# Optimization experiments

Hardware: AMD Instinct MI355X
Metric: run time of the kernel (lower is better)

## Reference

```python
import jax, jax.numpy as jnp
import numpy as np

B, M, D, V = 2048, 64, 256, 50000  # batch, max neighbors, embed dim, num_symbols (pad idx = V)
EPS = 1e-5


def _ln(x, g, b):
    mu = jnp.mean(x, axis=-1, keepdims=True)
    var = jnp.var(x, axis=-1, keepdims=True)
    return (x - mu) * jax.lax.rsqrt(var + EPS) * g + b


def _attn(q, k, v, Wq, Wk, Wv, Wb, Wo, bo):
    # q: (B, D); k, v: (B, M, D). num_heads=1, att_size=D. NOTE: self.scale is defined
    # but never used in the original forward, so no scaling here (faithful).
    qh = q @ Wq.T                                   # (B, D)
    kh = jnp.einsum('bmd,ed->bme', k, Wk)           # (B, M, D)
    vh = jnp.einsum('bmd,ed->bme', v, Wv)           # (B, M, D)
    s = jnp.einsum('bd,bmd->bm', qh @ Wb.T, kh)     # bilinear-modulated scores
    a = jax.nn.softmax(s, axis=-1)
    o = jnp.einsum('bm,bmd->bd', a, vh)
    return o @ Wo.T + bo


def setup_inputs() -> dict:
    key = jax.random.key(0)
    ks = jax.random.split(key, 40)
    f = lambda i, shape, s=0.05: (jax.random.normal(ks[i], shape, dtype=jnp.float32) * s)
    emb = f(0, (V + 1, D), 0.1).at[V].set(0.0)  # padding_idx row is zero
    inp = {
        'entity_pairs': jax.random.randint(ks[1], (B, 2), 0, V),
        'left_conn': jax.random.randint(ks[2], (B, M, 2), 0, V),
        'left_deg': jax.random.randint(ks[3], (B,), 0, M),
        'right_conn': jax.random.randint(ks[4], (B, M, 2), 0, V),
        'right_deg': jax.random.randint(ks[5], (B,), 0, M),
        'emb': emb,
        # task-aware attention params
        'Wq_t': f(6, (D, D)), 'Wk_t': f(7, (D, D)), 'Wv_t': f(8, (D, D)),
        'Wbil_t': f(9, (D, D)), 'Wo_t': f(10, (D, D)), 'bo_t': jnp.zeros((D,), jnp.float32),
        # entity-pair attention params
        'Wq_e': f(11, (D, D)), 'Wk_e': f(12, (D, D)), 'Wv_e': f(13, (D, D)),
        'Wbil_e': f(14, (D, D)), 'Wo_e': f(15, (D, D)), 'bo_e': jnp.zeros((D,), jnp.float32),
        'ln_g': jnp.ones((D,), jnp.float32), 'ln_b': jnp.zeros((D,), jnp.float32),
        'Wtail': f(16, (D, D)), 'Whead': f(17, (D, D)),
        'Wrel': f(18, (2 * D, D, D), 0.02),  # nn.Bilinear weight (out, in1, in2), no bias
        'W1': f(19, (2 * D, 2 * D)), 'b1': jnp.zeros((2 * D,), jnp.float32),
        'W2': f(20, (2 * D, 2 * D)),
        'ln1_g': jnp.ones((2 * D,), jnp.float32), 'ln1_b': jnp.zeros((2 * D,), jnp.float32),
        'Wg': f(21, (D, D), 0.3), 'Ug': f(22, (D, D), 0.3), 'bg': jnp.zeros((D,), jnp.float32),
        'Wr': f(23, (D, D), 0.3), 'Ur': f(24, (D, D), 0.3), 'br': jnp.zeros((D,), jnp.float32),
    }
    return inp


def reference(entity_pairs, left_conn, left_deg, right_conn, right_deg, emb,
              Wq_t, Wk_t, Wv_t, Wbil_t, Wo_t, bo_t,
              Wq_e, Wk_e, Wv_e, Wbil_e, Wo_e, bo_e,
              ln_g, ln_b, Wtail, Whead, Wrel, W1, b1, W2, ln1_g, ln1_b,
              Wg, Ug, bg, Wr, Ur, br):
    # eval mode: dropouts are identity
    ent = emb[entity_pairs]                 # (B, 2, D)
    eL, eR = ent[:, 0], ent[:, 1]           # (B, D) each
    rel_L = emb[left_conn[:, :, 0]]         # (B, M, D)
    ent_L = emb[left_conn[:, :, 1]]
    rel_R = emb[right_conn[:, :, 0]]
    ent_R = emb[right_conn[:, :, 1]]

    # rel_w bilinear: (B, 2D) -> split into forward/backward task relation embeddings
    rel_emb = jnp.einsum('bi,oij,bj->bo', eL, Wrel, eR)
    rel_fwd, rel_bwd = rel_emb[:, :D], rel_emb[:, D:]

    # GRU-style neighbor gating
    g = jax.nn.sigmoid(rel_L @ Wg + ent_L @ Ug + bg)
    V_head = jax.nn.relu(g * rel_L + (1.0 - g) * ent_L)
    gr = jax.nn.sigmoid(rel_R @ Wr + ent_R @ Ur + br)
    V_tail = jax.nn.relu(gr * rel_R + (1.0 - gr) * ent_R)

    def enhance(att_out, e):
        h = jax.nn.relu(att_out @ Wtail.T + e @ Whead.T)
        return _ln(h + e, ln_g, ln_b)

    h_rel = _attn(rel_fwd, rel_L, V_head, Wq_t, Wk_t, Wv_t, Wbil_t, Wo_t, bo_t)
    enh_head_ = enhance(h_rel, eL)
    t_rel = _attn(rel_bwd, rel_R, V_tail, Wq_t, Wk_t, Wv_t, Wbil_t, Wo_t, bo_t)
    enh_tail_ = enhance(t_rel, eR)

    h_ent = _attn(enh_tail_, ent_L, V_head, Wq_e, Wk_e, Wv_e, Wbil_e, Wo_e, bo_e)
    enh_head = enhance(h_ent, eL)
    t_ent = _attn(enh_head_, ent_R, V_tail, Wq_e, Wk_e, Wv_e, Wbil_e, Wo_e, bo_e)
    enh_tail = enhance(t_ent, eR)

    pair = jnp.concatenate([enh_head, enh_tail], axis=-1)  # (B, 2D)
    # bi_MLP with residual + LayerNorm
    h = jax.nn.relu(pair @ W1.T + b1)
    h = h @ W2.T
    return _ln(h + pair, ln1_g, ln1_b)
```

## Files before the change

kernel.cpp:

```cpp
#include <hip/hip_runtime.h>
#include <hip/hip_bf16.h>

#define BN 2048
#define MN 64
#define DN 256
#define EMB_ROWS 50001
#define EMB_PAD 50016
#define LN_EPS 1e-5f
#define SPLITK 16
#define KCHUNK 4096

typedef __hip_bfloat16 bf16;
typedef __attribute__((ext_vector_type(8))) short bf16x8;
typedef __attribute__((ext_vector_type(4))) float f32x4;

static __device__ __forceinline__ short f2bf(float f) {
  return __builtin_bit_cast(short, __float2bfloat16(f));
}
static __device__ __forceinline__ float bfu(unsigned short u) {
  unsigned int x = ((unsigned int)u) << 16;
  return __builtin_bit_cast(float, x);
}

typedef __attribute__((address_space(1))) const void g_void;
typedef __attribute__((address_space(3))) void l_void;
static __device__ __forceinline__ void gl_lds16(const void* g, void* l) {
  __builtin_amdgcn_global_load_lds((g_void*)g, (l_void*)l, 16, 0, 0);
}

static __device__ __forceinline__ void dev_mm(float* __restrict__ C, const float* __restrict__ A,
                                              const float* __restrict__ B, int N, int K,
                                              int aI, int aM, int bM, int bJ, int blk, int tid) {
  int idx = blk * 256 + tid;
  int i = idx / N, j = idx - i * N;
  float s = 0.f;
  for (int m = 0; m < K; ++m) s += A[i * aI + m * aM] * B[m * bM + j * bJ];
  C[idx] = s;
}
static __device__ __forceinline__ void dev_tr(float* __restrict__ dst, const float* __restrict__ src,
                                              int rows, int cols, int blk, int tid) {
  int idx = blk * 256 + tid;
  int r = idx / cols, c = idx - r * cols;
  dst[c * rows + r] = src[idx];
}

#define S1_GRID 27349
__global__ void k_stage1(const float* __restrict__ Wbil_t, const float* __restrict__ Wq_t,
                         const float* __restrict__ Wbil_e, const float* __restrict__ Wq_e,
                         const float* __restrict__ Wo_t, const float* __restrict__ Wv_t,
                         const float* __restrict__ Wo_e, const float* __restrict__ Wv_e,
                         const float* __restrict__ Wtail, const float* __restrict__ Whead,
                         const float* __restrict__ W1, const float* __restrict__ W2,
                         const float* __restrict__ Wg, const float* __restrict__ Ug,
                         const float* __restrict__ Wr, const float* __restrict__ Ur,
                         const float* __restrict__ Wrel, const float* __restrict__ emb,
                         const int* __restrict__ pairs,
                         float* __restrict__ T_t, float* __restrict__ T_e,
                         float* __restrict__ Wov_t, float* __restrict__ Wov_e,
                         float* __restrict__ WtailT, float* __restrict__ Whead_kn,
                         float* __restrict__ W1_kn, float* __restrict__ W2_kn,
                         bf16* __restrict__ wcat, bf16* __restrict__ emb_bf,
                         float* __restrict__ eL, float* __restrict__ eR,
                         bf16* __restrict__ eRbf, float* __restrict__ eLT,
                         bf16* __restrict__ Wrel_bf) {
  int bid = blockIdx.x, tid = threadIdx.x;
  if (bid < 256)        dev_mm(T_t, Wbil_t, Wq_t, 256, 256, 256, 1, 256, 1, bid, tid);
  else if (bid < 512)   dev_mm(T_e, Wbil_e, Wq_e, 256, 256, 256, 1, 256, 1, bid - 256, tid);
  else if (bid < 768)   dev_mm(Wov_t, Wo_t, Wv_t, 256, 256, 256, 1, 256, 1, bid - 512, tid);
  else if (bid < 1024)  dev_mm(Wov_e, Wo_e, Wv_e, 256, 256, 256, 1, 256, 1, bid - 768, tid);
  else if (bid < 1280)  dev_tr(WtailT, Wtail, 256, 256, bid - 1024, tid);
  else if (bid < 1536)  dev_tr(Whead_kn, Whead, 256, 256, bid - 1280, tid);
  else if (bid < 2560)  dev_tr(W1_kn, W1, 512, 512, bid - 1536, tid);
  else if (bid < 3584)  dev_tr(W2_kn, W2, 512, 512, bid - 2560, tid);
  else if (bid < 4608) {
    int idx = (bid - 3584) * 256 + tid;
    int n = idx >> 8, k = idx & 255;
    const float* s = (n < 256) ? Wg : (n < 512) ? Ug : (n < 768) ? Wr : Ur;
    wcat[idx] = __float2bfloat16(s[k * 256 + (n & 255)]);
  } else if (bid < 17109) {
    int i = (bid - 4608) * 256 + tid;
    if (i < (EMB_ROWS * 256) / 4) {
      float4 v = ((const float4*)emb)[i];
      ushort4 o;
      o.x = (unsigned short)f2bf(v.x); o.y = (unsigned short)f2bf(v.y);
      o.z = (unsigned short)f2bf(v.z); o.w = (unsigned short)f2bf(v.w);
      ((ushort4*)emb_bf)[i] = o;
    }
  } else if (bid < 19157) {
    int b = bid - 17109, d = tid;
    float vL = emb[(size_t)pairs[2 * b] * 256 + d];
    float vR = emb[(size_t)pairs[2 * b + 1] * 256 + d];
    eL[b * 256 + d] = vL;
    eR[b * 256 + d] = vR;
    eRbf[b * 256 + d] = __float2bfloat16(vR);
    eLT[(size_t)d * BN + b] = vL;
  } else {
    int blk = bid - 19157;
    int base = blk * 1024 + tid;
    #pragma unroll
    for (int it = 0; it < 4; ++it) {
      int i = base + it * 256;
      float4 v = ((const float4*)Wrel)[i];
      ushort4 o;
      o.x = (unsigned short)f2bf(v.x); o.y = (unsigned short)f2bf(v.y);
      o.z = (unsigned short)f2bf(v.z); o.w = (unsigned short)f2bf(v.w);
      ((ushort4*)Wrel_bf)[i] = o;
    }
  }
}

__global__ __launch_bounds__(256, 2) void k_bilinear(const bf16* __restrict__ eRbf,
                                                     const float* __restrict__ eLT,
                                                     const bf16* __restrict__ wrel,
                                                     float* __restrict__ part) {
  __shared__ char bsh[2][8192];
  int bid = blockIdx.x;
  int lid = (bid & 7) * 256 + (bid >> 3);
  int bx = lid & 15, by = (lid >> 4) & 7, bz = lid >> 7;
  int tid = threadIdx.x, w = tid >> 6, lane = tid & 63;
  int l16 = lane & 15, lq = lane >> 4;
  int kfo = lq * 8;
  int m_base = bx * 128 + w * 32;
  int n0 = by * 64;
  int i0 = bz * 16;

  bf16x8 ar[2][8];
  #pragma unroll
  for (int mi = 0; mi < 2; ++mi) {
    const bf16* er = eRbf + (size_t)(m_base + mi * 16 + l16) * 256 + kfo;
    #pragma unroll
    for (int jb = 0; jb < 8; ++jb) ar[mi][jb] = *(const bf16x8*)(er + jb * 32);
  }

  f32x4 z = {0.f, 0.f, 0.f, 0.f};
  f32x4 accF[2][4];
  f32x4 P[2][4];
  #pragma unroll
  for (int mi = 0; mi < 2; ++mi)
    #pragma unroll
    for (int nf = 0; nf < 4; ++nf) { accF[mi][nf] = z; P[mi][nf] = z; }

  int srow = tid >> 3, sblk = tid & 7;
  const bf16* wbase = wrel + (size_t)n0 * 65536 + (size_t)i0 * 256;
  auto stage = [&](int c, int step) {
    size_t so = (size_t)step * 64;
    #pragma unroll
    for (int q = 0; q < 2; ++q) {
      int r = q * 32 + srow;
      const bf16* src = wbase + (size_t)r * 65536 + so + (size_t)((sblk ^ (r & 7)) << 3);
      gl_lds16(src, &bsh[c][q * 4096 + w * 1024]);
    }
  };

  stage(0, 0);
  __syncthreads();
  int cur = 0;
  for (int s = 0; s < 16; ++s) {
    const float* elb = eLT + (size_t)(i0 + s) * BN + m_base + lq * 4;
    float4 el0 = *(const float4*)(elb);
    float4 el1 = *(const float4*)(elb + 16);
    #pragma unroll
    for (int jb4 = 0; jb4 < 4; ++jb4) {
      int step = s * 4 + jb4;
      if (step + 1 < 64) stage(cur ^ 1, step + 1);
      bf16x8 bq[2][4];
      #pragma unroll
      for (int kk = 0; kk < 2; ++kk)
        #pragma unroll
        for (int nf = 0; nf < 4; ++nf) {
          int rl = nf * 16 + l16;
          int blk = (kk * 4 + lq) ^ (l16 & 7);
          bq[kk][nf] = *(const bf16x8*)&bsh[cur][rl * 128 + (blk << 4)];
        }
      #pragma unroll
      for (int kk = 0; kk < 2; ++kk)
        #pragma unroll
        for (int mi = 0; mi < 2; ++mi)
          #pragma unroll
          for (int nf = 0; nf < 4; ++nf) {
            if (jb4 == 0 && kk == 0)
              P[mi][nf] = __builtin_amdgcn_mfma_f32_16x16x32_bf16(ar[mi][jb4 * 2 + kk], bq[kk][nf], z, 0, 0, 0);
            else
              P[mi][nf] = __builtin_amdgcn_mfma_f32_16x16x32_bf16(ar[mi][jb4 * 2 + kk], bq[kk][nf], P[mi][nf], 0, 0, 0);
          }
      __syncthreads();
      cur ^= 1;
    }
    #pragma unroll
    for (int mi = 0; mi < 2; ++mi) {
      float4 el = mi ? el1 : el0;
      #pragma unroll
      for (int nf = 0; nf < 4; ++nf) {
        accF[mi][nf][0] += el.x * P[mi][nf][0];
        accF[mi][nf][1] += el.y * P[mi][nf][1];
        accF[mi][nf][2] += el.z * P[mi][nf][2];
        accF[mi][nf][3] += el.w * P[mi][nf][3];
      }
    }
  }

  float* p = part + (size_t)bz * BN * 512;
  #pragma unroll
  for (int mi = 0; mi < 2; ++mi) {
    #pragma unroll
    for (int nf = 0; nf < 4; ++nf) {
      int col = n0 + nf * 16 + l16;
      #pragma unroll
      for (int r = 0; r < 4; ++r) {
        int row = m_base + mi * 16 + lq * 4 + r;
        p[(size_t)row * 512 + col] = accF[mi][nf][r];
      }
    }
  }
}

static __device__ __forceinline__ void dev_e4(char* wsh, int bid, const bf16* __restrict__ embbf,
                                              const bf16* __restrict__ wcat, bf16* __restrict__ E4) {
  int lid = (bid & 7) * 392 + (bid >> 3);
  int mchunk = lid >> 4, nt = lid & 15;
  int tid = threadIdx.x;
  int w = tid >> 6, lane = tid & 63;
  int l16 = lane & 15, lq = lane >> 4, kfo = lq * 8;
  int n0 = nt * 64;

  #pragma unroll
  for (int issue = 0; issue < 8; ++issue) {
    int L = issue * 4096 + tid * 16;
    int rl = L >> 9;
    int c  = (L >> 4) & 31;
    const char* src = (const char*)(wcat + (size_t)(n0 + rl) * 256) + ((c ^ (rl & 7)) << 4);
    gl_lds16(src, wsh + L);
  }
  __syncthreads();

  f32x4 z = {0.f, 0.f, 0.f, 0.f};
  #pragma unroll
  for (int g = 0; g < 4; ++g) {
    int rbase = mchunk * 256 + w * 64 + g * 16;
    int arow = rbase + l16; if (arow >= EMB_ROWS) arow = EMB_ROWS - 1;
    const bf16* ap = embbf + (size_t)arow * 256 + kfo;
    bf16x8 A[8];
    #pragma unroll
    for (int ks = 0; ks < 8; ++ks) A[ks] = *(const bf16x8*)(ap + ks * 32);
    f32x4 acc[4];
    #pragma unroll
    for (int nf = 0; nf < 4; ++nf) acc[nf] = z;
    #pragma unroll
    for (int ks = 0; ks < 8; ++ks) {
      bf16x8 bq[4];
      #pragma unroll
      for (int nf = 0; nf < 4; ++nf) {
        int rl = nf * 16 + l16;
        int c0 = ks * 4 + lq;
        bq[nf] = *(const bf16x8*)&wsh[rl * 512 + ((c0 ^ (rl & 7)) << 4)];
      }
      acc[0] = __builtin_amdgcn_mfma_f32_16x16x32_bf16(A[ks], bq[0], acc[0], 0, 0, 0);
      acc[1] = __builtin_amdgcn_mfma_f32_16x16x32_bf16(A[ks], bq[1], acc[1], 0, 0, 0);
      acc[2] = __builtin_amdgcn_mfma_f32_16x16x32_bf16(A[ks], bq[2], acc[2], 0, 0, 0);
      acc[3] = __builtin_amdgcn_mfma_f32_16x16x32_bf16(A[ks], bq[3], acc[3], 0, 0, 0);
    }
    #pragma unroll
    for (int nf = 0; nf < 4; ++nf) {
      int col = n0 + nf * 16 + l16;
      #pragma unroll
      for (int r = 0; r < 4; ++r) {
        int row = rbase + lq * 4 + r;
        if (row < EMB_ROWS) E4[(size_t)row * 1024 + col] = __float2bfloat16(acc[nf][r]);
      }
    }
  }
}

__global__ __launch_bounds__(256, 4) void k_e4s2(const bf16* __restrict__ embbf, const bf16* __restrict__ wcat,
                                                 bf16* __restrict__ E4,
                                                 const float* __restrict__ T_t, const float* __restrict__ Wk_t,
                                                 float* __restrict__ Cq_t,
                                                 const float* __restrict__ T_e, const float* __restrict__ Wk_e,
                                                 float* __restrict__ Cq_e,
                                                 const float* __restrict__ Wov_t, const float* __restrict__ WtailT,
                                                 float* __restrict__ Wenh_t,
                                                 const float* __restrict__ Wov_e, float* __restrict__ Wenh_e,
                                                 const float* __restrict__ Wtail, const float* __restrict__ bo_t,
                                                 const float* __restrict__ bo_e,
                                                 float* __restrict__ benh_t, float* __restrict__ benh_e) {
  __shared__ char wsh[32768];
  int bid = blockIdx.x, tid = threadIdx.x;
  if (bid < 3136) {
    dev_e4(wsh, bid, embbf, wcat, E4);
    return;
  }
  int b2 = bid - 3136;
  if (b2 < 256)       dev_mm(Cq_t, T_t, Wk_t, 256, 256, 1, 256, 256, 1, b2, tid);
  else if (b2 < 512)  dev_mm(Cq_e, T_e, Wk_e, 256, 256, 1, 256, 256, 1, b2 - 256, tid);
  else if (b2 < 768)  dev_mm(Wenh_t, Wov_t, WtailT, 256, 256, 1, 256, 256, 1, b2 - 512, tid);
  else if (b2 < 1024) dev_mm(Wenh_e, Wov_e, WtailT, 256, 256, 1, 256, 256, 1, b2 - 768, tid);
  else {
    float s1 = 0.f, s2 = 0.f;
    for (int m = 0; m < 256; ++m) {
      float wv = Wtail[tid * 256 + m];
      s1 += wv * bo_t[m];
      s2 += wv * bo_e[m];
    }
    benh_t[tid] = s1;
    benh_e[tid] = s2;
  }
}

static __device__ __forceinline__ void dev_vbuild(int bid, const int* __restrict__ lconn,
                                                  const int* __restrict__ rconn,
                                                  const bf16* __restrict__ embbf, const bf16* __restrict__ E4,
                                                  const float* __restrict__ bg, const float* __restrict__ br,
                                                  bf16* __restrict__ Vh, bf16* __restrict__ Vt) {
  int task = bid * 4 + (threadIdx.x >> 6);
  int lane = threadIdx.x & 63;
  int d0 = lane * 4;
  {
    int i0 = lconn[2 * task], i1 = lconn[2 * task + 1];
    ushort4 ga = *(const ushort4*)(E4 + (size_t)i0 * 1024 + d0);
    ushort4 gb = *(const ushort4*)(E4 + (size_t)i1 * 1024 + 256 + d0);
    float4 bgv = *(const float4*)(bg + d0);
    ushort4 ea = *(const ushort4*)(embbf + (size_t)i0 * 256 + d0);
    ushort4 eb = *(const ushort4*)(embbf + (size_t)i1 * 256 + d0);
    ushort4 oh;
    {
      float g = 1.f / (1.f + expf(-(bfu(ga.x) + bfu(gb.x) + bgv.x)));
      oh.x = (unsigned short)f2bf(fmaxf(g * bfu(ea.x) + (1.f - g) * bfu(eb.x), 0.f));
      g = 1.f / (1.f + expf(-(bfu(ga.y) + bfu(gb.y) + bgv.y)));
      oh.y = (unsigned short)f2bf(fmaxf(g * bfu(ea.y) + (1.f - g) * bfu(eb.y), 0.f));
      g = 1.f / (1.f + expf(-(bfu(ga.z) + bfu(gb.z) + bgv.z)));
      oh.z = (unsigned short)f2bf(fmaxf(g * bfu(ea.z) + (1.f - g) * bfu(eb.z), 0.f));
      g = 1.f / (1.f + expf(-(bfu(ga.w) + bfu(gb.w) + bgv.w)));
      oh.w = (unsigned short)f2bf(fmaxf(g * bfu(ea.w) + (1.f - g) * bfu(eb.w), 0.f));
    }
    *(ushort4*)(Vh + (size_t)task * 256 + d0) = oh;
  }
  {
    int r0 = rconn[2 * task], r1 = rconn[2 * task + 1];
    ushort4 ga = *(const ushort4*)(E4 + (size_t)r0 * 1024 + 512 + d0);
    ushort4 gb = *(const ushort4*)(E4 + (size_t)r1 * 1024 + 768 + d0);
    float4 brv = *(const float4*)(br + d0);
    ushort4 ea = *(const ushort4*)(embbf + (size_t)r0 * 256 + d0);
    ushort4 eb = *(const ushort4*)(embbf + (size_t)r1 * 256 + d0);
    ushort4 ot;
    {
      float g = 1.f / (1.f + expf(-(bfu(ga.x) + bfu(gb.x) + brv.x)));
      ot.x = (unsigned short)f2bf(fmaxf(g * bfu(ea.x) + (1.f - g) * bfu(eb.x), 0.f));
      g = 1.f / (1.f + expf(-(bfu(ga.y) + bfu(gb.y) + brv.y)));
      ot.y = (unsigned short)f2bf(fmaxf(g * bfu(ea.y) + (1.f - g) * bfu(eb.y), 0.f));
      g = 1.f / (1.f + expf(-(bfu(ga.z) + bfu(gb.z) + brv.z)));
      ot.z = (unsigned short)f2bf(fmaxf(g * bfu(ea.z) + (1.f - g) * bfu(eb.z), 0.f));
      g = 1.f / (1.f + expf(-(bfu(ga.w) + bfu(gb.w) + brv.w)));
      ot.w = (unsigned short)f2bf(fmaxf(g * bfu(ea.w) + (1.f - g) * bfu(eb.w), 0.f));
    }
    *(ushort4*)(Vt + (size_t)task * 256 + d0) = ot;
  }
}

__global__ __launch_bounds__(256) void k_vq(const int* __restrict__ lconn, const int* __restrict__ rconn,
                                            const bf16* __restrict__ embbf, const bf16* __restrict__ E4,
                                            const float* __restrict__ bg, const float* __restrict__ br,
                                            bf16* __restrict__ Vh, bf16* __restrict__ Vt,
                                            const float* __restrict__ part, const float* __restrict__ Cq,
                                            float* __restrict__ qkb) {
  __shared__ float xs[16][256];
  int bid = blockIdx.x, tid = threadIdx.x;
  if (bid < 32768) {
    dev_vbuild(bid, lconn, rconn, embbf, E4, bg, br, Vh, Vt);
    return;
  }
  int b2 = bid - 32768;
  int half = b2 >> 7;
  int r0 = (b2 & 127) * 16;
  int col0 = half * 256;
  for (int t = tid; t < 16 * 256; t += 256) {
    int r = t >> 8, k = t & 255;
    const float* pp = part + (size_t)(r0 + r) * 512 + col0 + k;
    float s = 0.f;
    #pragma unroll
    for (int zc = 0; zc < SPLITK; ++zc) s += pp[(size_t)zc * BN * 512];
    xs[r][k] = s;
  }
  __syncthreads();
  float acc[16];
  #pragma unroll
  for (int r = 0; r < 16; ++r) acc[r] = 0.f;
  for (int k4 = 0; k4 < 256; k4 += 4) {
    float w0 = Cq[(k4 + 0) * 256 + tid];
    float w1 = Cq[(k4 + 1) * 256 + tid];
    float w2 = Cq[(k4 + 2) * 256 + tid];
    float w3 = Cq[(k4 + 3) * 256 + tid];
    #pragma unroll
    for (int r = 0; r < 16; ++r) {
      float4 a = *(const float4*)&xs[r][k4];
      acc[r] += a.x * w0 + a.y * w1 + a.z * w2 + a.w * w3;
    }
  }
  int ob = half * 2048 + r0;
  #pragma unroll
  for (int r = 0; r < 16; ++r) qkb[(size_t)(ob + r) * 256 + tid] = acc[r];
}

__global__ __launch_bounds__(256) void k_qk34(const float* __restrict__ X0, const float* __restrict__ X1,
                                              const float* __restrict__ Cq, float* __restrict__ qkb) {
  __shared__ float xs[16][256];
  int bid = blockIdx.x, tid = threadIdx.x;
  int half = bid >> 7;
  const float* X = half ? X1 : X0;
  int r0 = (bid & 127) * 16;
  for (int t = tid; t < 16 * 256; t += 256) {
    int r = t >> 8, k = t & 255;
    xs[r][k] = X[(size_t)(r0 + r) * 256 + k];
  }
  __syncthreads();
  float acc[16];
  #pragma unroll
  for (int r = 0; r < 16; ++r) acc[r] = 0.f;
  for (int k4 = 0; k4 < 256; k4 += 4) {
    float w0 = Cq[(k4 + 0) * 256 + tid];
    float w1 = Cq[(k4 + 1) * 256 + tid];
    float w2 = Cq[(k4 + 2) * 256 + tid];
    float w3 = Cq[(k4 + 3) * 256 + tid];
    #pragma unroll
    for (int r = 0; r < 16; ++r) {
      float4 a = *(const float4*)&xs[r][k4];
      acc[r] += a.x * w0 + a.y * w1 + a.z * w2 + a.w * w3;
    }
  }
  int ob = half * 2048 + r0;
  #pragma unroll
  for (int r = 0; r < 16; ++r) qkb[(size_t)(ob + r) * 256 + tid] = acc[r];
}

__global__ __launch_bounds__(256) void k_attn_dual(const float* __restrict__ qk,
                                                   const int* __restrict__ lconn, const int* __restrict__ rconn,
                                                   const bf16* __restrict__ Vh, const bf16* __restrict__ Vt,
                                                   int sel, const bf16* __restrict__ embbf,
                                                   float* __restrict__ ov) {
  __shared__ float ss[64];
  __shared__ float as[64];
  __shared__ float ps[4][256];
  int bid = blockIdx.x;
  int b = bid & 2047;
  const int* conn = (bid < 2048) ? lconn : rconn;
  const bf16* Vbuf = (bid < 2048) ? Vh : Vt;
  int tid = threadIdx.x;
  int w = tid >> 6, lane = tid & 63;
  float4 qv = *(const float4*)(qk + (size_t)bid * 256 + lane * 4);
  for (int mi = 0; mi < 16; ++mi) {
    int m = w * 16 + mi;
    int idx = conn[((size_t)b * 64 + m) * 2 + sel];
    ushort4 kr = *(const ushort4*)(embbf + (size_t)idx * 256 + lane * 4);
    float p = qv.x * bfu(kr.x) + qv.y * bfu(kr.y) + qv.z * bfu(kr.z) + qv.w * bfu(kr.w);
    #pragma unroll
    for (int off = 32; off; off >>= 1) p += __shfl_xor(p, off, 64);
    if (lane == 0) ss[m] = p;
  }
  __syncthreads();
  if (w == 0) {
    float v = ss[lane];
    float mx = v;
    #pragma unroll
    for (int off = 32; off; off >>= 1) mx = fmaxf(mx, __shfl_xor(mx, off, 64));
    float e = expf(v - mx);
    float sum = e;
    #pragma unroll
    for (int off = 32; off; off >>= 1) sum += __shfl_xor(sum, off, 64);
    as[lane] = e / sum;
  }
  __syncthreads();
  const bf16* vrow = Vbuf + (size_t)b * 64 * 256;
  float4 a4 = {0.f, 0.f, 0.f, 0.f};
  for (int mi = 0; mi < 16; ++mi) {
    int m = w * 16 + mi;
    float sc = as[m];
    ushort4 v4 = *(const ushort4*)(vrow + (size_t)m * 256 + lane * 4);
    a4.x += sc * bfu(v4.x);
    a4.y += sc * bfu(v4.y);
    a4.z += sc * bfu(v4.z);
    a4.w += sc * bfu(v4.w);
  }
  *(float4*)&ps[w][lane * 4] = a4;
  __syncthreads();
  float o = ps[0][tid] + ps[1][tid] + ps[2][tid] + ps[3][tid];
  ov[(size_t)bid * 256 + tid] = o;
}

__global__ __launch_bounds__(256) void k_enh_dual(const float* __restrict__ ovb,
                                                  const float* __restrict__ e0, const float* __restrict__ e1,
                                                  const float* __restrict__ Wenh_kn, const float* __restrict__ Whead_kn,
                                                  const float* __restrict__ benh, const float* __restrict__ lng,
                                                  const float* __restrict__ lnb,
                                                  float* __restrict__ out0, float* __restrict__ out1,
                                                  int ostride, int ob0, int ob1) {
  __shared__ float x1[16][256];
  __shared__ float x2[16][256];
  __shared__ float stats[16][2];
  int bid = blockIdx.x, tid = threadIdx.x;
  int half = bid >> 7;
  const float* e = half ? e1 : e0;
  float* outp = half ? out1 : out0;
  int obase = half ? ob1 : ob0;
  int r0 = (bid & 127) * 16;
  int ovr0 = half * 2048 + r0;
  for (int t = tid; t < 16 * 256; t += 256) {
    int r = t >> 8, k = t & 255;
    x1[r][k] = ovb[(size_t)(ovr0 + r) * 256 + k];
    x2[r][k] = e[(size_t)(r0 + r) * 256 + k];
  }
  __syncthreads();
  float acc[16];
  #pragma unroll
  for (int r = 0; r < 16; ++r) acc[r] = 0.f;
  for (int k4 = 0; k4 < 256; k4 += 4) {
    float w10 = Wenh_kn[(k4 + 0) * 256 + tid], w11 = Wenh_kn[(k4 + 1) * 256 + tid];
    float w12 = Wenh_kn[(k4 + 2) * 256 + tid], w13 = Wenh_kn[(k4 + 3) * 256 + tid];
    float w20 = Whead_kn[(k4 + 0) * 256 + tid], w21 = Whead_kn[(k4 + 1) * 256 + tid];
    float w22 = Whead_kn[(k4 + 2) * 256 + tid], w23 = Whead_kn[(k4 + 3) * 256 + tid];
    #pragma unroll
    for (int r = 0; r < 16; ++r) {
      float4 a = *(const float4*)&x1[r][k4];
      float4 bb = *(const float4*)&x2[r][k4];
      acc[r] += a.x * w10 + a.y * w11 + a.z * w12 + a.w * w13
              + bb.x * w20 + bb.y * w21 + bb.z * w22 + bb.w * w23;
    }
  }
  float bz = benh[tid];
  float hv[16];
  #pragma unroll
  for (int r = 0; r < 16; ++r) hv[r] = fmaxf(acc[r] + bz, 0.f) + x2[r][tid];
  __syncthreads();
  #pragma unroll
  for (int r = 0; r < 16; ++r) x1[r][tid] = hv[r];
  __syncthreads();
  int w = tid >> 6, lane = tid & 63;
  for (int rr = 0; rr < 4; ++rr) {
    int r = w * 4 + rr;
    float s1 = 0.f, s2 = 0.f;
    #pragma unroll
    for (int jj = 0; jj < 4; ++jj) {
      float v = x1[r][lane + jj * 64];
      s1 += v; s2 += v * v;
    }
    #pragma unroll
    for (int off = 32; off; off >>= 1) {
      s1 += __shfl_xor(s1, off, 64);
      s2 += __shfl_xor(s2, off, 64);
    }
    if (lane == 0) {
      float mu = s1 * (1.f / 256.f);
      float var = s2 * (1.f / 256.f) - mu * mu;
      stats[r][0] = mu;
      stats[r][1] = rsqrtf(var + LN_EPS);
    }
  }
  __syncthreads();
  float gv = lng[tid], bv = lnb[tid];
  #pragma unroll
  for (int r = 0; r < 16; ++r) {
    float v = (x1[r][tid] - stats[r][0]) * stats[r][1] * gv + bv;
    outp[(size_t)(r0 + r) * ostride + obase + tid] = v;
  }
}

__global__ __launch_bounds__(256) void k_lin(const float* __restrict__ X, const float* __restrict__ Wkn,
                                             const float* __restrict__ bias, float* __restrict__ Y,
                                             int Kdim, int Ndim, int act) {
  __shared__ float xs[16][512];
  int tid = threadIdx.x;
  int r0 = blockIdx.x * 16;
  int col = blockIdx.y * 256 + tid;
  for (int t = tid; t < 16 * Kdim; t += 256) {
    int r = t / Kdim, k = t - r * Kdim;
    xs[r][k] = X[(size_t)(r0 + r) * Kdim + k];
  }
  __syncthreads();
  float acc[16];
  #pragma unroll
  for (int r = 0; r < 16; ++r) acc[r] = 0.f;
  for (int k4 = 0; k4 < Kdim; k4 += 4) {
    float w0 = Wkn[(size_t)(k4 + 0) * Ndim + col];
    float w1 = Wkn[(size_t)(k4 + 1) * Ndim + col];
    float w2 = Wkn[(size_t)(k4 + 2) * Ndim + col];
    float w3 = Wkn[(size_t)(k4 + 3) * Ndim + col];
    #pragma unroll
    for (int r = 0; r < 16; ++r) {
      float4 a = *(const float4*)&xs[r][k4];
      acc[r] += a.x * w0 + a.y * w1 + a.z * w2 + a.w * w3;
    }
  }
  float bv = bias ? bias[col] : 0.f;
  #pragma unroll
  for (int r = 0; r < 16; ++r) {
    float v = acc[r] + bv;
    if (act) v = fmaxf(v, 0.f);
    Y[(size_t)(r0 + r) * Ndim + col] = v;
  }
}

__global__ __launch_bounds__(256) void k_mlp2ln(const float* __restrict__ h1, const float* __restrict__ W2kn,
                                                const float* __restrict__ pairb, const float* __restrict__ g,
                                                const float* __restrict__ bb, float* __restrict__ out) {
  __shared__ float xs[16][512];
  __shared__ float stats[16][2];
  int bid = blockIdx.x, tid = threadIdx.x;
  int r0 = bid * 16;
  for (int t = tid; t < 16 * 512; t += 256) {
    int r = t >> 9, k = t & 511;
    xs[r][k] = h1[(size_t)(r0 + r) * 512 + k];
  }
  __syncthreads();
  float acc0[16], acc1[16];
  #pragma unroll
  for (int r = 0; r < 16; ++r) { acc0[r] = 0.f; acc1[r] = 0.f; }
  for (int k4 = 0; k4 < 512; k4 += 4) {
    float a0 = W2kn[(size_t)(k4 + 0) * 512 + tid];
    float a1 = W2kn[(size_t)(k4 + 1) * 512 + tid];
    float a2 = W2kn[(size_t)(k4 + 2) * 512 + tid];
    float a3 = W2kn[(size_t)(k4 + 3) * 512 + tid];
    float b0 = W2kn[(size_t)(k4 + 0) * 512 + tid + 256];
    float b1 = W2kn[(size_t)(k4 + 1) * 512 + tid + 256];
    float b2 = W2kn[(size_t)(k4 + 2) * 512 + tid + 256];
    float b3 = W2kn[(size_t)(k4 + 3) * 512 + tid + 256];
    #pragma unroll
    for (int r = 0; r < 16; ++r) {
      float4 a = *(const float4*)&xs[r][k4];
      acc0[r] += a.x * a0 + a.y * a1 + a.z * a2 + a.w * a3;
      acc1[r] += a.x * b0 + a.y * b1 + a.z * b2 + a.w * b3;
    }
  }
  __syncthreads();
  #pragma unroll
  for (int r = 0; r < 16; ++r) {
    xs[r][tid]       = acc0[r] + pairb[(size_t)(r0 + r) * 512 + tid];
    xs[r][tid + 256] = acc1[r] + pairb[(size_t)(r0 + r) * 512 + tid + 256];
  }
  __syncthreads();
  int w = tid >> 6, lane = tid & 63;
  for (int rr = 0; rr < 4; ++rr) {
    int r = w * 4 + rr;
    float s1 = 0.f, s2 = 0.f;
    #pragma unroll
    for (int jj = 0; jj < 8; ++jj) {
      float v = xs[r][lane + jj * 64];
      s1 += v; s2 += v * v;
    }
    #pragma unroll
    for (int off = 32; off; off >>= 1) {
      s1 += __shfl_xor(s1, off, 64);
      s2 += __shfl_xor(s2, off, 64);
    }
    if (lane == 0) {
      float mu = s1 * (1.f / 512.f);
      stats[r][0] = mu;
      stats[r][1] = rsqrtf(s2 * (1.f / 512.f) - mu * mu + LN_EPS);
    }
  }
  __syncthreads();
  float g0 = g[tid], g1 = g[tid + 256], b0v = bb[tid], b1v = bb[tid + 256];
  #pragma unroll
  for (int r = 0; r < 16; ++r) {
    float mu = stats[r][0], rstd = stats[r][1];
    out[(size_t)(r0 + r) * 512 + tid]       = (xs[r][tid] - mu) * rstd * g0 + b0v;
    out[(size_t)(r0 + r) * 512 + tid + 256] = (xs[r][tid + 256] - mu) * rstd * g1 + b1v;
  }
}

extern "C" void kernel_launch(void* const* d_in, const int* in_sizes, int n_in,
                              void* d_out, int out_size, void* d_ws, size_t ws_size,
                              hipStream_t stream) {
  (void)in_sizes; (void)n_in; (void)out_size; (void)ws_size;
  const int*   entity_pairs = (const int*)d_in[0];
  const int*   left_conn    = (const int*)d_in[1];
  const int*   right_conn   = (const int*)d_in[3];
  const float* emb    = (const float*)d_in[5];
  const float* Wq_t   = (const float*)d_in[6];
  const float* Wk_t   = (const float*)d_in[7];
  const float* Wv_t   = (const float*)d_in[8];
  const float* Wbil_t = (const float*)d_in[9];
  const float* Wo_t   = (const float*)d_in[10];
  const float* bo_t   = (const float*)d_in[11];
  const float* Wq_e   = (const float*)d_in[12];
  const float* Wk_e   = (const float*)d_in[13];
  const float* Wv_e   = (const float*)d_in[14];
  const float* Wbil_e = (const float*)d_in[15];
  const float* Wo_e   = (const float*)d_in[16];
  const float* bo_e   = (const float*)d_in[17];
  const float* ln_g   = (const float*)d_in[18];
  const float* ln_b   = (const float*)d_in[19];
  const float* Wtail  = (const float*)d_in[20];
  const float* Whead  = (const float*)d_in[21];
  const float* Wrel   = (const float*)d_in[22];
  const float* W1     = (const float*)d_in[23];
  const float* b1     = (const float*)d_in[24];
  const float* W2     = (const float*)d_in[25];
  const float* ln1_g  = (const float*)d_in[26];
  const float* ln1_b  = (const float*)d_in[27];
  const float* Wg     = (const float*)d_in[28];
  const float* Ug     = (const float*)d_in[29];
  const float* bg     = (const float*)d_in[30];
  const float* Wr     = (const float*)d_in[31];
  const float* Ur     = (const float*)d_in[32];
  const float* br     = (const float*)d_in[33];
  float* out = (float*)d_out;

  char* wp = (char*)d_ws;
  auto alloc = [&](size_t bytes) -> void* {
    void* p = (void*)wp;
    wp += (bytes + 255) & ~(size_t)255;
    return p;
  };
  bf16* Wrel_bf = (bf16*)alloc((size_t)512 * 65536 * 2);
  bf16* emb_bf  = (bf16*)alloc((size_t)EMB_PAD * 256 * 2);
  bf16* E4      = (bf16*)alloc((size_t)EMB_PAD * 1024 * 2);
  bf16* wcat    = (bf16*)alloc((size_t)1024 * 256 * 2);
  bf16* Vh      = (bf16*)alloc((size_t)BN * MN * 256 * 2);
  bf16* Vt      = (bf16*)alloc((size_t)BN * MN * 256 * 2);
  bf16* eRbf_g  = (bf16*)alloc((size_t)BN * 256 * 2);
  float* eLT    = (float*)alloc((size_t)256 * BN * 4);
  float* eLp     = (float*)alloc((size_t)BN * 256 * 4);
  float* eRp     = (float*)alloc((size_t)BN * 256 * 4);
  float* bil_part= (float*)alloc((size_t)SPLITK * BN * 512 * 4);
  float* qkbuf   = (float*)alloc((size_t)2 * BN * 256 * 4);
  float* ovbuf   = (float*)alloc((size_t)2 * BN * 256 * 4);
  float* enh_h   = (float*)alloc((size_t)BN * 256 * 4);
  float* enh_t   = (float*)alloc((size_t)BN * 256 * 4);
  float* pairb   = (float*)alloc((size_t)BN * 512 * 4);
  float* h1buf   = (float*)alloc((size_t)BN * 512 * 4);
  float* T_t     = (float*)alloc(256 * 256 * 4);
  float* Cq_t    = (float*)alloc(256 * 256 * 4);
  float* Wov_t   = (float*)alloc(256 * 256 * 4);
  float* Wenh_t  = (float*)alloc(256 * 256 * 4);
  float* benh_t  = (float*)alloc(256 * 4);
  float* T_e     = (float*)alloc(256 * 256 * 4);
  float* Cq_e    = (float*)alloc(256 * 256 * 4);
  float* Wov_e   = (float*)alloc(256 * 256 * 4);
  float* Wenh_e  = (float*)alloc(256 * 256 * 4);
  float* benh_e  = (float*)alloc(256 * 4);
  float* Whead_kn= (float*)alloc(256 * 256 * 4);
  float* WtailT  = (float*)alloc(256 * 256 * 4);
  float* W1_kn   = (float*)alloc(512 * 512 * 4);
  float* W2_kn   = (float*)alloc(512 * 512 * 4);

  k_stage1<<<S1_GRID, 256, 0, stream>>>(Wbil_t, Wq_t, Wbil_e, Wq_e, Wo_t, Wv_t, Wo_e, Wv_e,
                                        Wtail, Whead, W1, W2, Wg, Ug, Wr, Ur, Wrel, emb,
                                        entity_pairs,
                                        T_t, T_e, Wov_t, Wov_e, WtailT, Whead_kn, W1_kn, W2_kn,
                                        wcat, emb_bf, eLp, eRp, eRbf_g, eLT, Wrel_bf);
  k_bilinear<<<2048, 256, 0, stream>>>(eRbf_g, eLT, Wrel_bf, bil_part);
  k_e4s2<<<4161, 256, 0, stream>>>(emb_bf, wcat, E4,
                                   T_t, Wk_t, Cq_t, T_e, Wk_e, Cq_e,
                                   Wov_t, WtailT, Wenh_t, Wov_e, Wenh_e,
                                   Wtail, bo_t, bo_e, benh_t, benh_e);
  k_vq<<<33024, 256, 0, stream>>>(left_conn, right_conn, emb_bf, E4, bg, br, Vh, Vt,
                                  bil_part, Cq_t, qkbuf);
  k_attn_dual<<<4096, 256, 0, stream>>>(qkbuf, left_conn, right_conn, Vh, Vt, 0, emb_bf, ovbuf);
  k_enh_dual<<<256, 256, 0, stream>>>(ovbuf, eLp, eRp, Wenh_t, Whead_kn, benh_t, ln_g, ln_b,
                                      enh_h, enh_t, 256, 0, 0);
  k_qk34<<<256, 256, 0, stream>>>(enh_t, enh_h, Cq_e, qkbuf);
  k_attn_dual<<<4096, 256, 0, stream>>>(qkbuf, left_conn, right_conn, Vh, Vt, 1, emb_bf, ovbuf);
  k_enh_dual<<<256, 256, 0, stream>>>(ovbuf, eLp, eRp, Wenh_e, Whead_kn, benh_e, ln_g, ln_b,
                                      pairb, pairb, 512, 0, 256);

  k_lin<<<dim3(128, 2), 256, 0, stream>>>(pairb, W1_kn, b1, h1buf, 512, 512, 1);
  k_mlp2ln<<<128, 256, 0, stream>>>(h1buf, W2_kn, pairb, ln1_g, ln1_b, out);
}
```

Baseline: 962.6 us.

## Stage E4 tile epilogue through LDS for vectorized 16-byte stores

The E4 projection kernel now writes its MFMA accumulators into a per-wave padded LDS staging buffer and reads them back as 8-element bf16 vectors, so each global store is 16 bytes instead of scattered 2-byte writes. The weight-tile LDS layout is reorganized into four K-quarter planes with a smaller XOR swizzle to match the new read pattern. Launch bounds drop from 4 to 2 blocks per CU to make room for the extra shared memory, which can reduce occupancy.

```diff
diff --git a/kernel.cpp b/kernel.cpp
--- a/kernel.cpp
+++ b/kernel.cpp
@@ -214,7 +214,8 @@
   }
 }
 
-static __device__ __forceinline__ void dev_e4(char* wsh, int bid, const bf16* __restrict__ embbf,
+static __device__ __forceinline__ void dev_e4(char* wsh, char* tb, int bid,
+                                              const bf16* __restrict__ embbf,
                                               const bf16* __restrict__ wcat, bf16* __restrict__ E4) {
   int lid = (bid & 7) * 392 + (bid >> 3);
   int mchunk = lid >> 4, nt = lid & 15;
@@ -226,13 +227,16 @@
   #pragma unroll
   for (int issue = 0; issue < 8; ++issue) {
     int L = issue * 4096 + tid * 16;
-    int rl = L >> 9;
-    int c  = (L >> 4) & 31;
-    const char* src = (const char*)(wcat + (size_t)(n0 + rl) * 256) + ((c ^ (rl & 7)) << 4);
+    int q = L >> 13;
+    int rl = (L >> 7) & 63;
+    int blk = (L >> 4) & 7;
+    const bf16* src = wcat + (size_t)(n0 + rl) * 256 + q * 64 + ((blk ^ (rl & 7)) << 3);
     gl_lds16(src, wsh + L);
   }
   __syncthreads();
 
+  char* tw = tb + w * 2176;
+  int trow = lane >> 2, tc = lane & 3;
   f32x4 z = {0.f, 0.f, 0.f, 0.f};
   #pragma unroll
   for (int g = 0; g < 4; ++g) {
@@ -247,12 +251,13 @@
     for (int nf = 0; nf < 4; ++nf) acc[nf] = z;
     #pragma unroll
     for (int ks = 0; ks < 8; ++ks) {
+      int qd = ks >> 1, kk = ks & 1;
       bf16x8 bq[4];
       #pragma unroll
       for (int nf = 0; nf < 4; ++nf) {
         int rl = nf * 16 + l16;
-        int c0 = ks * 4 + lq;
-        bq[nf] = *(const bf16x8*)&wsh[rl * 512 + ((c0 ^ (rl & 7)) << 4)];
+        int blk = (kk * 4 + lq) ^ (l16 & 7);
+        bq[nf] = *(const bf16x8*)&wsh[qd * 8192 + rl * 128 + (blk << 4)];
       }
       acc[0] = __builtin_amdgcn_mfma_f32_16x16x32_bf16(A[ks], bq[0], acc[0], 0, 0, 0);
       acc[1] = __builtin_amdgcn_mfma_f32_16x16x32_bf16(A[ks], bq[1], acc[1], 0, 0, 0);
@@ -260,18 +265,21 @@
       acc[3] = __builtin_amdgcn_mfma_f32_16x16x32_bf16(A[ks], bq[3], acc[3], 0, 0, 0);
     }
     #pragma unroll
-    for (int nf = 0; nf < 4; ++nf) {
-      int col = n0 + nf * 16 + l16;
+    for (int nf = 0; nf < 4; ++nf)
       #pragma unroll
-      for (int r = 0; r < 4; ++r) {
-        int row = rbase + lq * 4 + r;
-        if (row < EMB_ROWS) E4[(size_t)row * 1024 + col] = __float2bfloat16(acc[nf][r]);
-      }
-    }
-  }
-}
-
-__global__ __launch_bounds__(256, 4) void k_e4s2(const bf16* __restrict__ embbf, const bf16* __restrict__ wcat,
+      for (int r = 0; r < 4; ++r)
+        *(bf16*)(tw + (lq * 4 + r) * 136 + (nf * 16 + l16) * 2) = __float2bfloat16(acc[nf][r]);
+    int orow = rbase + trow;
+    #pragma unroll
+    for (int it = 0; it < 2; ++it) {
+      bf16x8 vv = *(const bf16x8*)(tw + trow * 136 + (tc + 4 * it) * 16);
+      if (orow < EMB_ROWS)
+        *(bf16x8*)(E4 + (size_t)orow * 1024 + n0 + (tc + 4 * it) * 8) = vv;
+    }
+  }
+}
+
+__global__ __launch_bounds__(256, 2) void k_e4s2(const bf16* __restrict__ embbf, const bf16* __restrict__ wcat,
                                                  bf16* __restrict__ E4,
                                                  const float* __restrict__ T_t, const float* __restrict__ Wk_t,
                                                  float* __restrict__ Cq_t,
@@ -283,10 +291,10 @@
                                                  const float* __restrict__ Wtail, const float* __restrict__ bo_t,
                                                  const float* __restrict__ bo_e,
                                                  float* __restrict__ benh_t, float* __restrict__ benh_e) {
-  __shared__ char wsh[32768];
+  __shared__ char wsh[32768 + 4 * 2176];
   int bid = blockIdx.x, tid = threadIdx.x;
   if (bid < 3136) {
-    dev_e4(wsh, bid, embbf, wcat, E4);
+    dev_e4(wsh, wsh + 32768, bid, embbf, wcat, E4);
     return;
   }
   int b2 = bid - 3136;
```

Result: faster. 902.9 us (-6.2%).
